# Kernel optimization log

Hardware: AMD Instinct MI355X
Metric: run time of the kernel (lower is better)

Reference implementation:

```python
import jax, jax.numpy as jnp
import numpy as np
import math

NUM_BUCKETS = 32
MAX_DISTANCE = 128

def _next_pow2(n):
    return 1 << (int(n) - 1).bit_length()

def _rel_pos_bucket(rel_pos):
    # causal T5 bucket: n = max(q - k, 0)
    n = jnp.maximum(-rel_pos, 0)
    max_exact = NUM_BUCKETS // 2
    is_small = n < max_exact
    n_safe = jnp.maximum(n, 1).astype(jnp.float32)
    val_if_large = max_exact + (
        jnp.log(n_safe / max_exact) / math.log(MAX_DISTANCE / max_exact) * (NUM_BUCKETS - max_exact)
    ).astype(jnp.int32)
    val_if_large = jnp.minimum(val_if_large, NUM_BUCKETS - 1)
    return jnp.where(is_small, n, val_if_large)

def setup_inputs() -> dict:
    key = jax.random.key(0)
    ks = jax.random.split(key, 20)
    B, L, D = 8, 2048, 128
    H, DQK, DV = 16, 64, 256
    s = 0.05
    return {
        'x': jax.random.normal(ks[0], (B, L, D), jnp.float32),
        'expansion': jax.random.normal(ks[1], (H, D), jnp.float32) * s,
        'reduction': jax.random.normal(ks[2], (H, D), jnp.float32) * s,
        'alphas': jax.random.normal(ks[3], (H,), jnp.float32),
        'dampen_factors': jax.random.normal(ks[4], (H,), jnp.float32),
        'rel_bias': jax.random.normal(ks[5], (NUM_BUCKETS, 1), jnp.float32) * s,
        'W_qk': jax.random.normal(ks[6], (D, DQK), jnp.float32) * s,
        'b_qk': jnp.zeros((DQK,), jnp.float32),
        'gamma': jax.random.normal(ks[7], (2, DQK), jnp.float32) * 0.02 + 1.0,
        'beta': jnp.zeros((2, DQK), jnp.float32),
        'W_v': jax.random.normal(ks[8], (D, DV), jnp.float32) * s,
        'b_v': jnp.zeros((DV,), jnp.float32),
        'W_reset': jax.random.normal(ks[9], (D, DV), jnp.float32) * s,
        'b_reset': jnp.zeros((DV,), jnp.float32),
        'W_update': jax.random.normal(ks[10], (D, D), jnp.float32) * s,
        'b_update': jnp.zeros((D,), jnp.float32),
        'Wh': jax.random.normal(ks[11], (D, D), jnp.float32) * s,
        'Uh': jax.random.normal(ks[12], (DV, D), jnp.float32) * s,
        'bh': jnp.zeros((D,), jnp.float32),
    }

def reference(x, expansion, reduction, alphas, dampen_factors, rel_bias,
              W_qk, b_qk, gamma, beta, W_v, b_v, W_reset, b_reset,
              W_update, b_update, Wh, Uh, bh):
    B, L, D = x.shape
    DQK = W_qk.shape[1]
    # ---- MultiHeadedEMA (causal, FFT conv) ----
    xe = jnp.einsum('bnd,hd->bnhd', x, expansion)  # [B,L,H,D]
    a = jax.nn.sigmoid(alphas)
    damp = jax.nn.sigmoid(dampen_factors)
    t = jnp.arange(L, dtype=x.dtype)
    kern = a[:, None] * ((1.0 - a) * damp)[:, None] ** t[None, :]  # [H,L]
    fft_len = _next_pow2(2 * L - 1)
    Xf = jnp.fft.rfft(xe, n=fft_len, axis=1)           # [B,F,H,D]
    Kf = jnp.fft.rfft(kern, n=fft_len, axis=-1)        # [H,F]
    y = jnp.fft.irfft(Xf * Kf.T[None, :, :, None], n=fft_len, axis=1)[:, :L]
    ema = jnp.einsum('bnhd,hd->bnd', y, reduction)     # [B,L,D]
    # ---- SingleHeadedAttention(ema, v_input=x) ----
    qk = jax.nn.silu(ema @ W_qk + b_qk)                # [B,L,DQK]
    q = qk * gamma[0] + beta[0]
    k = qk * gamma[1] + beta[1]
    v = jax.nn.silu(x @ W_v + b_v)                     # [B,L,DV]
    scale = D ** -0.5
    sim = jnp.einsum('bid,bjd->bij', q, k) * scale
    pos = jnp.arange(L)
    rel = pos[None, :] - pos[:, None]                  # [L,L] j - i
    bias = rel_bias[_rel_pos_bucket(rel), 0] * (DQK ** 0.5)
    sim = sim + bias
    sim = jnp.where(rel > 0, jnp.finfo(sim.dtype).min, sim)  # strict causal mask
    attn = jax.nn.softmax(sim, axis=-1)
    attn_out = jnp.einsum('bij,bjd->bid', attn, v)     # [B,L,DV]
    # ---- gating ----
    reset_gate = jax.nn.silu(ema @ W_reset + b_reset)
    update_gate = jax.nn.sigmoid(ema @ W_update + b_update)
    gated = attn_out * reset_gate
    Hh = jax.nn.silu(ema @ Wh + gated @ Uh + bh)
    return update_gate * Hh + (1.0 - update_gate) * x
```

## Files before the change

kernel.cpp:

```cpp
#include <hip/hip_runtime.h>
#include <hip/hip_bf16.h>
#include <math.h>

#define BB 8
#define LL 2048
#define DD 128
#define DQKN 64
#define DVN 256
#define MTOT (BB*LL)
#define SCALE 0.08838834764831845f
#define LOG2E 1.4426950408889634f
#define QSCALE (SCALE*LOG2E)

#define CHUNK 32
#define NCH (LL/CHUNK)
#define CT 4
#define NCHK 144

typedef __attribute__((ext_vector_type(4))) float f32x4;
typedef __attribute__((ext_vector_type(8))) short s16x8;

__device__ __forceinline__ float sigmoidf_(float x){ return 1.f/(1.f+__expf(-x)); }
__device__ __forceinline__ float siluf_(float x){ return x/(1.f+__expf(-x)); }
__device__ __forceinline__ __hip_bfloat16 f2bf(float f){ return __float2bfloat16(f); }
__device__ __forceinline__ ushort f2bfu(float f){ __hip_bfloat16 h = __float2bfloat16(f); return *(const ushort*)&h; }
__device__ __forceinline__ float bf2f(ushort u){ union{unsigned i; float f;} v; v.i = ((unsigned)u)<<16; return v.f; }

__device__ __forceinline__ void gl_lds16(const __hip_bfloat16* g, void* l) {
    __builtin_amdgcn_global_load_lds(
        (const __attribute__((address_space(1))) void*)g,
        (__attribute__((address_space(3))) void*)l, 16, 0, 0);
}

__global__ void pack_all(const float* __restrict__ Wqk, const float* __restrict__ Wv,
                         const float* __restrict__ Wrst, const float* __restrict__ Wu,
                         const float* __restrict__ Wh, const float* __restrict__ Uh,
                         const float* __restrict__ rel_bias,
                         __hip_bfloat16* __restrict__ WqkP, __hip_bfloat16* __restrict__ WvP,
                         __hip_bfloat16* __restrict__ WrstP, __hip_bfloat16* __restrict__ WuP,
                         __hip_bfloat16* __restrict__ WhP, __hip_bfloat16* __restrict__ UhP,
                         float* __restrict__ btab) {
    int blk = blockIdx.x;
    int l = threadIdx.x;
    if (blk == 272) {
        for (int n = l; n < LL; n += 64) {
            int bucket;
            if (n < 16) bucket = n;
            else {
                float v = logf((float)n * (1.0f/16.0f)) * (1.0f/logf(8.0f)) * 16.0f;
                bucket = 16 + (int)v;
                if (bucket > 31) bucket = 31;
            }
            btab[n] = rel_bias[bucket] * 8.0f * LOG2E;
        }
        return;
    }
    const float* W; __hip_bfloat16* Wp; int K, N;
    if (blk < 16)       { W=Wqk;  Wp=WqkP;  K=128; N=64; }
    else if (blk < 80)  { W=Wv;   Wp=WvP;   K=128; N=256; blk-=16; }
    else if (blk < 144) { W=Wrst; Wp=WrstP; K=128; N=256; blk-=80; }
    else if (blk < 176) { W=Wu;   Wp=WuP;   K=128; N=128; blk-=144; }
    else if (blk < 208) { W=Wh;   Wp=WhP;   K=128; N=128; blk-=176; }
    else                { W=Uh;   Wp=UhP;   K=256; N=128; blk-=208; }
    int k32 = blk % (K/32), n16 = blk / (K/32);
    int col = n16*16 + (l & 15);
    int krow = k32*32 + (l >> 4)*8;
    ushort tmp[8];
    #pragma unroll
    for (int j = 0; j < 8; ++j) tmp[j] = f2bfu(W[(size_t)(krow + j)*N + col]);
    *reinterpret_cast<uint4*>(Wp + ((size_t)blk*64 + l)*8) = *reinterpret_cast<uint4*>(tmp);
}

__global__ __launch_bounds__(256) void ema_scanA(const float* __restrict__ x,
                                                 const float* __restrict__ alphas,
                                                 const float* __restrict__ damps,
                                                 float* __restrict__ sl,
                                                 __hip_bfloat16* __restrict__ xb) {
    int tid = blockIdx.x * 256 + threadIdx.x;
    int d = tid & 127;
    int c = (tid >> 7) & (NCH - 1);
    int b = tid >> 13;
    float u[16], r[16];
    #pragma unroll
    for (int h = 0; h < 16; ++h) {
        float a = sigmoidf_(alphas[h]);
        r[h] = (1.f - a) * sigmoidf_(damps[h]);
        u[h] = 0.f;
    }
    const float* xp = x + ((size_t)b * LL + c * CHUNK) * DD + d;
    __hip_bfloat16* xbp = xb + ((size_t)b * LL + c * CHUNK) * DD + d;
    #pragma unroll 4
    for (int i = 0; i < CHUNK; ++i) {
        float xv = xp[(size_t)i * DD];
        xbp[(size_t)i * DD] = f2bf(xv);
        #pragma unroll
        for (int h = 0; h < 16; ++h) u[h] = fmaf(r[h], u[h], xv);
    }
    float* slp = sl + ((size_t)b * NCH + c) * 16 * DD + d;
    #pragma unroll
    for (int h = 0; h < 16; ++h) slp[(size_t)h * DD] = u[h];
}

__global__ __launch_bounds__(256) void ema_scanB(const float* __restrict__ alphas,
                                                 const float* __restrict__ damps,
                                                 const float* __restrict__ sl,
                                                 float* __restrict__ carry) {
    int tid = blockIdx.x * 256 + threadIdx.x;
    int d = tid & 127;
    int h = (tid >> 7) & 15;
    int b = tid >> 11;
    float a = sigmoidf_(alphas[h]);
    float r = (1.f - a) * sigmoidf_(damps[h]);
    float rC = r;
    #pragma unroll
    for (int q = 0; q < 5; ++q) rC *= rC;
    const float* slp = sl + ((size_t)b * NCH * 16 + h) * DD + d;
    float* cp = carry + ((size_t)b * NCH * 16 + h) * DD + d;
    float u = 0.f;
    #pragma unroll 8
    for (int c = 0; c < NCH; ++c) {
        cp[(size_t)c * 16 * DD] = u;
        u = slp[(size_t)c * 16 * DD] + rC * u;
    }
}

__global__ __launch_bounds__(256) void ema_scanC(const __hip_bfloat16* __restrict__ xb,
                                                 const float* __restrict__ expansion,
                                                 const float* __restrict__ reduction,
                                                 const float* __restrict__ alphas,
                                                 const float* __restrict__ damps,
                                                 const float* __restrict__ carry,
                                                 __hip_bfloat16* __restrict__ emab) {
    int tid = blockIdx.x * 256 + threadIdx.x;
    int d = tid & 127;
    int c = (tid >> 7) & (NCH - 1);
    int b = tid >> 13;
    float u[16], r[16], we[16];
    #pragma unroll
    for (int h = 0; h < 16; ++h) {
        float a = sigmoidf_(alphas[h]);
        r[h] = (1.f - a) * sigmoidf_(damps[h]);
        we[h] = reduction[h * DD + d] * a * expansion[h * DD + d];
        u[h] = carry[((size_t)b * NCH + c) * 16 * DD + (size_t)h * DD + d];
    }
    const __hip_bfloat16* xp = xb + ((size_t)b * LL + c * CHUNK) * DD + d;
    __hip_bfloat16* ep = emab + ((size_t)b * LL + c * CHUNK) * DD + d;
    #pragma unroll 4
    for (int i = 0; i < CHUNK; ++i) {
        float xv = __bfloat162float(xp[(size_t)i * DD]);
        float acc = 0.f;
        #pragma unroll
        for (int h = 0; h < 16; ++h) {
            u[h] = fmaf(r[h], u[h], xv);
            acc = fmaf(we[h], u[h], acc);
        }
        ep[(size_t)i * DD] = f2bf(acc);
    }
}

__global__ __launch_bounds__(256) void gemm_fused(const __hip_bfloat16* __restrict__ xb,
        const __hip_bfloat16* __restrict__ emab,
        const __hip_bfloat16* __restrict__ WvP, const __hip_bfloat16* __restrict__ WrstP,
        const __hip_bfloat16* __restrict__ WqkP,
        const float* __restrict__ b_v, const float* __restrict__ b_rst,
        const float* __restrict__ b_qk, const float* __restrict__ gamma,
        const float* __restrict__ beta,
        __hip_bfloat16* __restrict__ vT, __hip_bfloat16* __restrict__ rstb,
        __hip_bfloat16* __restrict__ qb, __hip_bfloat16* __restrict__ kb) {
    __shared__ char AsB[64*256];
    const int mode = blockIdx.y;
    const __hip_bfloat16* A = (mode == 0) ? xb : emab;
    const int row0 = blockIdx.x * 64;
    const int t = threadIdx.x, w = t>>6, lane = t&63, l16 = lane&15, l4 = lane>>4;
    #pragma unroll
    for (int p = 0; p < 4; ++p) {
        int idx = p*256 + t;
        int row = idx / 16, u = idx % 16;
        uint4 d = *reinterpret_cast<const uint4*>(A + (size_t)(row0+row)*DD + u*8);
        *reinterpret_cast<uint4*>(AsB + row*256 + ((u*16) ^ ((row&7)<<4))) = d;
    }
    __syncthreads();
    const int arow = w*16 + l16;
    if (mode == 2) {
        f32x4 acc[4];
        #pragma unroll
        for (int n = 0; n < 4; ++n) acc[n] = (f32x4){0.f,0.f,0.f,0.f};
        #pragma unroll
        for (int k32 = 0; k32 < 4; ++k32) {
            s16x8 af = *reinterpret_cast<const s16x8*>(AsB + arow*256 + ((k32*64 + l4*16) ^ ((arow&7)<<4)));
            #pragma unroll
            for (int n = 0; n < 4; ++n) {
                s16x8 bfr = *reinterpret_cast<const s16x8*>(WqkP + ((size_t)(n*4 + k32)*64 + lane)*8);
                acc[n] = __builtin_amdgcn_mfma_f32_16x16x32_bf16(af, bfr, acc[n], 0, 0, 0);
            }
        }
        #pragma unroll
        for (int n = 0; n < 4; ++n) {
            int col = n*16 + l16;
            float bb = b_qk[col];
            float g0 = gamma[col], g1 = gamma[DQKN + col];
            float be0 = beta[col], be1 = beta[DQKN + col];
            #pragma unroll
            for (int r = 0; r < 4; ++r) {
                int row = w*16 + l4*4 + r;
                float s = siluf_(acc[n][r] + bb);
                qb[(size_t)(row0+row)*DQKN + col] = f2bf((s*g0 + be0) * QSCALE);
                kb[(size_t)(row0+row)*DQKN + col] = f2bf(s*g1 + be1);
            }
        }
        return;
    }
    const __hip_bfloat16* Wp = mode ? WrstP : WvP;
    const float* bias = mode ? b_rst : b_v;
    f32x4 acc[16];
    #pragma unroll
    for (int n = 0; n < 16; ++n) acc[n] = (f32x4){0.f,0.f,0.f,0.f};
    #pragma unroll
    for (int k32 = 0; k32 < 4; ++k32) {
        s16x8 af = *reinterpret_cast<const s16x8*>(AsB + arow*256 + ((k32*64 + l4*16) ^ ((arow&7)<<4)));
        #pragma unroll
        for (int n = 0; n < 16; ++n) {
            s16x8 bfr = *reinterpret_cast<const s16x8*>(Wp + ((size_t)(n*4 + k32)*64 + lane)*8);
            acc[n] = __builtin_amdgcn_mfma_f32_16x16x32_bf16(af, bfr, acc[n], 0, 0, 0);
        }
    }
    if (mode == 0) {
        int bb_i = row0 >> 11;
        int lpos0 = (row0 & 2047) + w*16 + l4*4;
        #pragma unroll
        for (int n = 0; n < 16; ++n) {
            int col = n*16 + l16;
            float bb = bias[col];
            ushort pk[4];
            #pragma unroll
            for (int r = 0; r < 4; ++r) pk[r] = f2bfu(siluf_(acc[n][r] + bb));
            *reinterpret_cast<ushort4*>(vT + ((size_t)bb_i*DVN + col)*LL + lpos0) = *reinterpret_cast<ushort4*>(pk);
        }
    } else {
        #pragma unroll
        for (int n = 0; n < 16; ++n) {
            int col = n*16 + l16;
            float bb = bias[col];
            #pragma unroll
            for (int r = 0; r < 4; ++r) {
                int row = w*16 + l4*4 + r;
                rstb[(size_t)(row0+row)*DVN + col] = f2bf(siluf_(acc[n][r] + bb));
            }
        }
    }
}

__global__ __launch_bounds__(256) void attn_kernel(
    const __hip_bfloat16* __restrict__ qg, const __hip_bfloat16* __restrict__ kg,
    const __hip_bfloat16* __restrict__ vTg, const float* __restrict__ btab,
    __hip_bfloat16* __restrict__ aob, __hip_bfloat16* __restrict__ part_o,
    float* __restrict__ part_ml) {
    __shared__ __hip_bfloat16 Ks[64 * 64];
    __shared__ __hip_bfloat16 Vs[256 * 64];
    __shared__ __hip_bfloat16 Ps[4][16][72];
    __shared__ float btl[320];
    const int cid = NCHK - 1 - (int)blockIdx.y;
    const int b = blockIdx.x;
    int g = 0;
    while (cid >= 2*(g+1)*(g+2)) ++g;
    const int rel = cid - 2*g*(g+1);
    const int ti = 4*g + rel/(g+1);
    const int cch = rel % (g+1);
    const int i0 = ti * 64;
    const int jlo = cch * (CT*64);
    int jhi = jlo + CT*64; { int je = (ti+1)*64; if (jhi > je) jhi = je; }
    const int nt = (jhi - jlo) >> 6;
    const int t = threadIdx.x;
    const int w = t >> 6, lane = t & 63;
    const int l16 = lane & 15, l4 = lane >> 4;
    char* KsB = (char*)Ks;
    char* VsB = (char*)Vs;

    int dmin = i0 - jhi + 1; if (dmin < 0) dmin = 0;
    const int cnt = (i0 + 63 - jlo) - dmin + 1;
    for (int idx = t; idx < cnt; idx += 256) btl[idx] = btab[dmin + idx];

    const int irow = i0 + w * 16 + l16;
    s16x8 qf[2];
    qf[0] = *reinterpret_cast<const s16x8*>(qg + ((size_t)b * LL + irow) * DQKN + l4 * 8);
    qf[1] = *reinterpret_cast<const s16x8*>(qg + ((size_t)b * LL + irow) * DQKN + 32 + l4 * 8);

    f32x4 o[16];
    #pragma unroll
    for (int n16 = 0; n16 < 16; ++n16) o[n16] = (f32x4){0.f, 0.f, 0.f, 0.f};
    float m[4] = {-1e30f, -1e30f, -1e30f, -1e30f};
    float l[4] = {0.f, 0.f, 0.f, 0.f};

    for (int tt = 0; tt < nt; ++tt) {
        const int j0 = jlo + tt * 64;
        __syncthreads();
        #pragma unroll
        for (int i = 0; i < 2; ++i) {
            int base = w * 128 + i * 64;
            int idx = base + lane;
            int row = idx >> 3;
            int c16 = (idx & 7) ^ (row & 7);
            gl_lds16(kg + ((size_t)b * LL + j0 + row) * DQKN + c16 * 8, KsB + base * 16);
        }
        #pragma unroll
        for (int i = 0; i < 8; ++i) {
            int base = w * 512 + i * 64;
            int idx = base + lane;
            int n = idx >> 3;
            int c16 = (idx & 7) ^ (n & 7);
            gl_lds16(vTg + ((size_t)b * DVN + n) * LL + j0 + c16 * 8, VsB + base * 16);
        }
        __syncthreads();
        f32x4 s[4];
        #pragma unroll
        for (int t16 = 0; t16 < 4; ++t16) s[t16] = (f32x4){0.f, 0.f, 0.f, 0.f};
        #pragma unroll
        for (int c = 0; c < 2; ++c) {
            #pragma unroll
            for (int t16 = 0; t16 < 4; ++t16) {
                int j = t16 * 16 + l16;
                s16x8 kf = *reinterpret_cast<const s16x8*>(KsB + j * 128 + ((c * 64 + l4 * 16) ^ ((j & 7) << 4)));
                s[t16] = __builtin_amdgcn_mfma_f32_16x16x32_bf16(qf[c], kf, s[t16], 0, 0, 0);
            }
        }
        float sv[4][4];
        float rmax[4] = {-1e30f, -1e30f, -1e30f, -1e30f};
        #pragma unroll
        for (int t16 = 0; t16 < 4; ++t16) {
            #pragma unroll
            for (int r = 0; r < 4; ++r) {
                int row = l4 * 4 + r;
                int dlt = (i0 + w * 16 + row) - (j0 + t16 * 16 + l16);
                int bi = dlt - dmin; if (bi < 0) bi = 0;
                float bv = btl[bi];
                float val = (dlt >= 0) ? (s[t16][r] + bv) : -1e30f;
                sv[t16][r] = val;
                rmax[r] = fmaxf(rmax[r], val);
            }
        }
        #pragma unroll
        for (int off = 1; off < 16; off <<= 1) {
            #pragma unroll
            for (int r = 0; r < 4; ++r) rmax[r] = fmaxf(rmax[r], __shfl_xor(rmax[r], off));
        }
        bool need = (rmax[0] > m[0]) || (rmax[1] > m[1]) || (rmax[2] > m[2]) || (rmax[3] > m[3]);
        if (__any(need)) {
            float alpha[4];
            #pragma unroll
            for (int r = 0; r < 4; ++r) {
                float mn = fmaxf(m[r], rmax[r]);
                alpha[r] = exp2f(m[r] - mn);
                m[r] = mn;
                l[r] *= alpha[r];
            }
            #pragma unroll
            for (int n16 = 0; n16 < 16; ++n16) {
                #pragma unroll
                for (int r = 0; r < 4; ++r) o[n16][r] *= alpha[r];
            }
        }
        float psum[4] = {0.f, 0.f, 0.f, 0.f};
        #pragma unroll
        for (int t16 = 0; t16 < 4; ++t16) {
            #pragma unroll
            for (int r = 0; r < 4; ++r) {
                float p = exp2f(sv[t16][r] - m[r]);
                psum[r] += p;
                Ps[w][l4 * 4 + r][t16 * 16 + l16] = f2bf(p);
            }
        }
        #pragma unroll
        for (int off = 1; off < 16; off <<= 1) {
            #pragma unroll
            for (int r = 0; r < 4; ++r) psum[r] += __shfl_xor(psum[r], off);
        }
        #pragma unroll
        for (int r = 0; r < 4; ++r) l[r] += psum[r];
        #pragma unroll
        for (int c = 0; c < 2; ++c) {
            s16x8 pf = *reinterpret_cast<const s16x8*>(&Ps[w][l16][c * 32 + l4 * 8]);
            #pragma unroll
            for (int n16 = 0; n16 < 16; ++n16) {
                int n = n16 * 16 + l16;
                s16x8 vf = *reinterpret_cast<const s16x8*>(VsB + n * 128 + ((c * 64 + l4 * 16) ^ ((n & 7) << 4)));
                o[n16] = __builtin_amdgcn_mfma_f32_16x16x32_bf16(pf, vf, o[n16], 0, 0, 0);
            }
        }
    }
    if (ti < 4) {
        float invl[4];
        #pragma unroll
        for (int r = 0; r < 4; ++r) invl[r] = 1.f / l[r];
        #pragma unroll
        for (int n16 = 0; n16 < 16; ++n16) {
            #pragma unroll
            for (int r = 0; r < 4; ++r) {
                aob[((size_t)b * LL + i0 + w * 16 + l4 * 4 + r) * DVN + n16 * 16 + l16] = f2bf(o[n16][r] * invl[r]);
            }
        }
    } else {
        const size_t slot = (size_t)b * NCHK + cid;
        __hip_bfloat16* po = part_o + slot * (64 * 256);
        #pragma unroll
        for (int n16 = 0; n16 < 16; ++n16) {
            #pragma unroll
            for (int r = 0; r < 4; ++r)
                po[(size_t)(w * 16 + l4 * 4 + r) * 256 + n16 * 16 + l16] = f2bf(o[n16][r]);
        }
        if (l16 == 0) {
            #pragma unroll
            for (int r = 0; r < 4; ++r) {
                int row = w * 16 + l4 * 4 + r;
                part_ml[slot * 128 + row * 2]     = m[r];
                part_ml[slot * 128 + row * 2 + 1] = l[r];
            }
        }
    }
}

__global__ __launch_bounds__(256) void attn_combine(const __hip_bfloat16* __restrict__ part_o,
                                                    const float* __restrict__ part_ml,
                                                    __hip_bfloat16* __restrict__ aob) {
    const int ti = 4 + (int)blockIdx.x;
    const int ch = blockIdx.y;
    const int b = blockIdx.z;
    const int g = ti >> 2;
    const int nc = g + 1;
    const int cid0 = 2*g*(g+1) + (ti - 4*g)*(g+1);
    const size_t slot0 = (size_t)b * NCHK + cid0;
    __shared__ float sW[8][64];
    __shared__ float sinvL[64];
    const int t = threadIdx.x;
    if (t < 64) {
        float M = -1e30f;
        for (int c = 0; c < nc; ++c)
            M = fmaxf(M, part_ml[(slot0 + c) * 128 + t * 2]);
        float L = 0.f;
        for (int c = 0; c < nc; ++c) {
            float wv = exp2f(part_ml[(slot0 + c) * 128 + t * 2] - M);
            sW[c][t] = wv;
            L += wv * part_ml[(slot0 + c) * 128 + t * 2 + 1];
        }
        sinvL[t] = 1.f / L;
    }
    __syncthreads();
    const int i0 = ti * 64;
    #pragma unroll
    for (int it = 0; it < 4; ++it) {
        int idx = it * 256 + t;
        int row = idx >> 4, c8 = idx & 15;
        int colu = ch * 16 + c8;
        float acc[8] = {0.f,0.f,0.f,0.f,0.f,0.f,0.f,0.f};
        for (int c = 0; c < nc; ++c) {
            float wv = sW[c][row];
            uint4 d = *reinterpret_cast<const uint4*>(part_o + (slot0 + c) * (size_t)(64*256) + row * 256 + colu * 8);
            const ushort* pp = (const ushort*)&d;
            #pragma unroll
            for (int j = 0; j < 8; ++j) acc[j] = fmaf(wv, bf2f(pp[j]), acc[j]);
        }
        float il = sinvL[row];
        ushort pk[8];
        #pragma unroll
        for (int j = 0; j < 8; ++j) pk[j] = f2bfu(acc[j] * il);
        *reinterpret_cast<uint4*>(aob + ((size_t)b * LL + i0 + row) * DVN + colu * 8) = *reinterpret_cast<uint4*>(pk);
    }
}

__global__ __launch_bounds__(256) void final_mfma(
        const __hip_bfloat16* __restrict__ emab, const __hip_bfloat16* __restrict__ aob,
        const __hip_bfloat16* __restrict__ rstb, const float* __restrict__ x,
        const __hip_bfloat16* __restrict__ WhP, const __hip_bfloat16* __restrict__ UhP,
        const __hip_bfloat16* __restrict__ WuP, const float* __restrict__ bh,
        const float* __restrict__ bu, float* __restrict__ out) {
    __shared__ char As1[64*256];
    __shared__ char As2[64*512];
    const int row0 = blockIdx.x * 64;
    const int ch = blockIdx.y;
    const int t = threadIdx.x, w = t>>6, lane = t&63, l16 = lane&15, l4 = lane>>4;
    #pragma unroll
    for (int p = 0; p < 4; ++p) {
        int idx = p*256 + t;
        int row = idx / 16, u = idx % 16;
        uint4 d = *reinterpret_cast<const uint4*>(emab + (size_t)(row0+row)*DD + u*8);
        *reinterpret_cast<uint4*>(As1 + row*256 + ((u*16) ^ ((row&7)<<4))) = d;
    }
    #pragma unroll
    for (int p = 0; p < 8; ++p) {
        int idx = p*256 + t;
        int row = idx / 32, u = idx % 32;
        uint4 da = *reinterpret_cast<const uint4*>(aob + (size_t)(row0+row)*DVN + u*8);
        uint4 dr = *reinterpret_cast<const uint4*>(rstb + (size_t)(row0+row)*DVN + u*8);
        const ushort* pa = (const ushort*)&da;
        const ushort* pr = (const ushort*)&dr;
        ushort gg[8];
        #pragma unroll
        for (int j = 0; j < 8; ++j) gg[j] = f2bfu(bf2f(pa[j]) * bf2f(pr[j]));
        *reinterpret_cast<uint4*>(As2 + row*512 + ((u*16) ^ ((row&7)<<4))) = *reinterpret_cast<uint4*>(gg);
    }
    __syncthreads();
    f32x4 acc1[4], acc2[4];
    #pragma unroll
    for (int n = 0; n < 4; ++n) { acc1[n] = (f32x4){0.f,0.f,0.f,0.f}; acc2[n] = (f32x4){0.f,0.f,0.f,0.f}; }
    const int arow = w*16 + l16;
    #pragma unroll
    for (int k32 = 0; k32 < 4; ++k32) {
        s16x8 af = *reinterpret_cast<const s16x8*>(As1 + arow*256 + ((k32*64 + l4*16) ^ ((arow&7)<<4)));
        #pragma unroll
        for (int n = 0; n < 4; ++n) {
            s16x8 bw = *reinterpret_cast<const s16x8*>(WhP + ((size_t)((ch*4+n)*4 + k32)*64 + lane)*8);
            acc1[n] = __builtin_amdgcn_mfma_f32_16x16x32_bf16(af, bw, acc1[n], 0, 0, 0);
            s16x8 bu2 = *reinterpret_cast<const s16x8*>(WuP + ((size_t)((ch*4+n)*4 + k32)*64 + lane)*8);
            acc2[n] = __builtin_amdgcn_mfma_f32_16x16x32_bf16(af, bu2, acc2[n], 0, 0, 0);
        }
    }
    #pragma unroll
    for (int k32 = 0; k32 < 8; ++k32) {
        s16x8 gf = *reinterpret_cast<const s16x8*>(As2 + arow*512 + ((k32*64 + l4*16) ^ ((arow&7)<<4)));
        #pragma unroll
        for (int n = 0; n < 4; ++n) {
            s16x8 bw = *reinterpret_cast<const s16x8*>(UhP + ((size_t)((ch*4+n)*8 + k32)*64 + lane)*8);
            acc1[n] = __builtin_amdgcn_mfma_f32_16x16x32_bf16(gf, bw, acc1[n], 0, 0, 0);
        }
    }
    #pragma unroll
    for (int n = 0; n < 4; ++n) {
        int col = ch*64 + n*16 + l16;
        float bbh = bh[col], bbu = bu[col];
        #pragma unroll
        for (int r = 0; r < 4; ++r) {
            int row = w*16 + l4*4 + r;
            size_t gidx = (size_t)(row0+row)*DD + col;
            float hh = siluf_(acc1[n][r] + bbh);
            float u = sigmoidf_(acc2[n][r] + bbu);
            float xv = x[gidx];
            out[gidx] = u*hh + (1.f-u)*xv;
        }
    }
}

extern "C" void kernel_launch(void* const* d_in, const int* in_sizes, int n_in,
                              void* d_out, int out_size, void* d_ws, size_t ws_size,
                              hipStream_t stream) {
    const float* x        = (const float*)d_in[0];
    const float* expansion= (const float*)d_in[1];
    const float* reduction= (const float*)d_in[2];
    const float* alphas   = (const float*)d_in[3];
    const float* damps    = (const float*)d_in[4];
    const float* rel_bias = (const float*)d_in[5];
    const float* W_qk     = (const float*)d_in[6];
    const float* b_qk     = (const float*)d_in[7];
    const float* gamma    = (const float*)d_in[8];
    const float* beta     = (const float*)d_in[9];
    const float* W_v      = (const float*)d_in[10];
    const float* b_v      = (const float*)d_in[11];
    const float* W_reset  = (const float*)d_in[12];
    const float* b_reset  = (const float*)d_in[13];
    const float* W_update = (const float*)d_in[14];
    const float* b_update = (const float*)d_in[15];
    const float* Wh       = (const float*)d_in[16];
    const float* Uh       = (const float*)d_in[17];
    const float* bh       = (const float*)d_in[18];
    float* out = (float*)d_out;

    char* base = (char*)d_ws;
    __hip_bfloat16* emab = (__hip_bfloat16*)base;  base += (size_t)MTOT * DD * 2;
    __hip_bfloat16* xb   = (__hip_bfloat16*)base;  base += (size_t)MTOT * DD * 2;
    __hip_bfloat16* qb   = (__hip_bfloat16*)base;  base += (size_t)MTOT * DQKN * 2;
    __hip_bfloat16* kb   = (__hip_bfloat16*)base;  base += (size_t)MTOT * DQKN * 2;
    __hip_bfloat16* vT   = (__hip_bfloat16*)base;  base += (size_t)MTOT * DVN * 2;
    __hip_bfloat16* rstb = (__hip_bfloat16*)base;  base += (size_t)MTOT * DVN * 2;
    __hip_bfloat16* aob  = (__hip_bfloat16*)base;  base += (size_t)MTOT * DVN * 2;
    float* btab  = (float*)base;                   base += (size_t)LL * 4;
    float* sl    = (float*)base;                   base += (size_t)BB * NCH * 16 * DD * 4;
    float* carry = (float*)base;                   base += (size_t)BB * NCH * 16 * DD * 4;
    __hip_bfloat16* WqkP = (__hip_bfloat16*)base;  base += (size_t)DD * DQKN * 2;
    __hip_bfloat16* WvP  = (__hip_bfloat16*)base;  base += (size_t)DD * DVN * 2;
    __hip_bfloat16* WrstP= (__hip_bfloat16*)base;  base += (size_t)DD * DVN * 2;
    __hip_bfloat16* WuP  = (__hip_bfloat16*)base;  base += (size_t)DD * DD * 2;
    __hip_bfloat16* WhP  = (__hip_bfloat16*)base;  base += (size_t)DD * DD * 2;
    __hip_bfloat16* UhP  = (__hip_bfloat16*)base;  base += (size_t)DVN * DD * 2;
    __hip_bfloat16* part_o = (__hip_bfloat16*)base; base += (size_t)BB * NCHK * 64 * 256 * 2;
    float* part_ml = (float*)base;                 base += (size_t)BB * NCHK * 128 * 4;

    pack_all<<<273, 64, 0, stream>>>(W_qk, W_v, W_reset, W_update, Wh, Uh, rel_bias,
                                     WqkP, WvP, WrstP, WuP, WhP, UhP, btab);

    ema_scanA<<<BB * NCH * DD / 256, 256, 0, stream>>>(x, alphas, damps, sl, xb);
    ema_scanB<<<BB * 16 * DD / 256, 256, 0, stream>>>(alphas, damps, sl, carry);
    ema_scanC<<<BB * NCH * DD / 256, 256, 0, stream>>>(xb, expansion, reduction, alphas, damps, carry, emab);

    gemm_fused<<<dim3(MTOT/64, 3), 256, 0, stream>>>(xb, emab, WvP, WrstP, WqkP,
                                                     b_v, b_reset, b_qk, gamma, beta,
                                                     vT, rstb, qb, kb);

    attn_kernel<<<dim3(BB, NCHK), 256, 0, stream>>>(qb, kb, vT, btab, aob, part_o, part_ml);
    attn_combine<<<dim3(28, 2, BB), 256, 0, stream>>>(part_o, part_ml, aob);

    final_mfma<<<dim3(MTOT/64, 2), 256, 0, stream>>>(emab, aob, rstb, x, WhP, UhP, WuP, bh, b_update, out);
}
```

Before: 117.8 us.

## Fuse attention combine into final GEMM and merge weight packing with scan

Removes the separate attn_combine kernel and the aob intermediate. Every attention tile, including the first four that used to normalize in place, now writes partials, and the final kernel merges the split-K partials while it builds the gated operand. The final kernel also computes all 128 output columns per block instead of splitting columns across two blocks, so the emab/gate staging is not duplicated. Weight packing and the first EMA scan pass are merged into one launch. Together these cut kernel launches and a full bf16 round trip of the attention output, at the cost of fewer final blocks and more register pressure per block.

```diff
diff --git a/kernel.cpp b/kernel.cpp
--- a/kernel.cpp
+++ b/kernel.cpp
@@ -32,50 +32,52 @@
         (__attribute__((address_space(3))) void*)l, 16, 0, 0);
 }
 
-__global__ void pack_all(const float* __restrict__ Wqk, const float* __restrict__ Wv,
-                         const float* __restrict__ Wrst, const float* __restrict__ Wu,
-                         const float* __restrict__ Wh, const float* __restrict__ Uh,
-                         const float* __restrict__ rel_bias,
-                         __hip_bfloat16* __restrict__ WqkP, __hip_bfloat16* __restrict__ WvP,
-                         __hip_bfloat16* __restrict__ WrstP, __hip_bfloat16* __restrict__ WuP,
-                         __hip_bfloat16* __restrict__ WhP, __hip_bfloat16* __restrict__ UhP,
-                         float* __restrict__ btab) {
-    int blk = blockIdx.x;
-    int l = threadIdx.x;
-    if (blk == 272) {
-        for (int n = l; n < LL; n += 64) {
-            int bucket;
-            if (n < 16) bucket = n;
-            else {
-                float v = logf((float)n * (1.0f/16.0f)) * (1.0f/logf(8.0f)) * 16.0f;
-                bucket = 16 + (int)v;
-                if (bucket > 31) bucket = 31;
-            }
-            btab[n] = rel_bias[bucket] * 8.0f * LOG2E;
-        }
+__global__ __launch_bounds__(256) void prep_kernel(
+        const float* __restrict__ x, const float* __restrict__ alphas,
+        const float* __restrict__ damps, float* __restrict__ sl,
+        __hip_bfloat16* __restrict__ xb,
+        const float* __restrict__ Wqk, const float* __restrict__ Wv,
+        const float* __restrict__ Wrst, const float* __restrict__ Wu,
+        const float* __restrict__ Wh, const float* __restrict__ Uh,
+        const float* __restrict__ rel_bias,
+        __hip_bfloat16* __restrict__ WqkP, __hip_bfloat16* __restrict__ WvP,
+        __hip_bfloat16* __restrict__ WrstP, __hip_bfloat16* __restrict__ WuP,
+        __hip_bfloat16* __restrict__ WhP, __hip_bfloat16* __restrict__ UhP,
+        float* __restrict__ btab) {
+    if (blockIdx.x >= 256) {
+        int sub = ((int)blockIdx.x - 256) * 4 + ((int)threadIdx.x >> 6);
+        int l = threadIdx.x & 63;
+        if (sub >= 273) return;
+        if (sub == 272) {
+            for (int n = l; n < LL; n += 64) {
+                int bucket;
+                if (n < 16) bucket = n;
+                else {
+                    float v = logf((float)n * (1.0f/16.0f)) * (1.0f/logf(8.0f)) * 16.0f;
+                    bucket = 16 + (int)v;
+                    if (bucket > 31) bucket = 31;
+                }
+                btab[n] = rel_bias[bucket] * 8.0f * LOG2E;
+            }
+            return;
+        }
+        int blk = sub;
+        const float* W; __hip_bfloat16* Wp; int K, N;
+        if (blk < 16)       { W=Wqk;  Wp=WqkP;  K=128; N=64; }
+        else if (blk < 80)  { W=Wv;   Wp=WvP;   K=128; N=256; blk-=16; }
+        else if (blk < 144) { W=Wrst; Wp=WrstP; K=128; N=256; blk-=80; }
+        else if (blk < 176) { W=Wu;   Wp=WuP;   K=128; N=128; blk-=144; }
+        else if (blk < 208) { W=Wh;   Wp=WhP;   K=128; N=128; blk-=176; }
+        else                { W=Uh;   Wp=UhP;   K=256; N=128; blk-=208; }
+        int k32 = blk % (K/32), n16 = blk / (K/32);
+        int col = n16*16 + (l & 15);
+        int krow = k32*32 + (l >> 4)*8;
+        ushort tmp[8];
+        #pragma unroll
+        for (int j = 0; j < 8; ++j) tmp[j] = f2bfu(W[(size_t)(krow + j)*N + col]);
+        *reinterpret_cast<uint4*>(Wp + ((size_t)blk*64 + l)*8) = *reinterpret_cast<uint4*>(tmp);
         return;
     }
-    const float* W; __hip_bfloat16* Wp; int K, N;
-    if (blk < 16)       { W=Wqk;  Wp=WqkP;  K=128; N=64; }
-    else if (blk < 80)  { W=Wv;   Wp=WvP;   K=128; N=256; blk-=16; }
-    else if (blk < 144) { W=Wrst; Wp=WrstP; K=128; N=256; blk-=80; }
-    else if (blk < 176) { W=Wu;   Wp=WuP;   K=128; N=128; blk-=144; }
-    else if (blk < 208) { W=Wh;   Wp=WhP;   K=128; N=128; blk-=176; }
-    else                { W=Uh;   Wp=UhP;   K=256; N=128; blk-=208; }
-    int k32 = blk % (K/32), n16 = blk / (K/32);
-    int col = n16*16 + (l & 15);
-    int krow = k32*32 + (l >> 4)*8;
-    ushort tmp[8];
-    #pragma unroll
-    for (int j = 0; j < 8; ++j) tmp[j] = f2bfu(W[(size_t)(krow + j)*N + col]);
-    *reinterpret_cast<uint4*>(Wp + ((size_t)blk*64 + l)*8) = *reinterpret_cast<uint4*>(tmp);
-}
-
-__global__ __launch_bounds__(256) void ema_scanA(const float* __restrict__ x,
-                                                 const float* __restrict__ alphas,
-                                                 const float* __restrict__ damps,
-                                                 float* __restrict__ sl,
-                                                 __hip_bfloat16* __restrict__ xb) {
     int tid = blockIdx.x * 256 + threadIdx.x;
     int d = tid & 127;
     int c = (tid >> 7) & (NCH - 1);
@@ -253,8 +255,7 @@
 __global__ __launch_bounds__(256) void attn_kernel(
     const __hip_bfloat16* __restrict__ qg, const __hip_bfloat16* __restrict__ kg,
     const __hip_bfloat16* __restrict__ vTg, const float* __restrict__ btab,
-    __hip_bfloat16* __restrict__ aob, __hip_bfloat16* __restrict__ part_o,
-    float* __restrict__ part_ml) {
+    __hip_bfloat16* __restrict__ part_o, float* __restrict__ part_ml) {
     __shared__ __hip_bfloat16 Ks[64 * 64];
     __shared__ __hip_bfloat16 Vs[256 * 64];
     __shared__ __hip_bfloat16 Ps[4][16][72];
@@ -387,50 +388,43 @@
             }
         }
     }
-    if (ti < 4) {
-        float invl[4];
-        #pragma unroll
-        for (int r = 0; r < 4; ++r) invl[r] = 1.f / l[r];
-        #pragma unroll
-        for (int n16 = 0; n16 < 16; ++n16) {
-            #pragma unroll
-            for (int r = 0; r < 4; ++r) {
-                aob[((size_t)b * LL + i0 + w * 16 + l4 * 4 + r) * DVN + n16 * 16 + l16] = f2bf(o[n16][r] * invl[r]);
-            }
-        }
-    } else {
-        const size_t slot = (size_t)b * NCHK + cid;
-        __hip_bfloat16* po = part_o + slot * (64 * 256);
-        #pragma unroll
-        for (int n16 = 0; n16 < 16; ++n16) {
-            #pragma unroll
-            for (int r = 0; r < 4; ++r)
-                po[(size_t)(w * 16 + l4 * 4 + r) * 256 + n16 * 16 + l16] = f2bf(o[n16][r]);
-        }
-        if (l16 == 0) {
-            #pragma unroll
-            for (int r = 0; r < 4; ++r) {
-                int row = w * 16 + l4 * 4 + r;
-                part_ml[slot * 128 + row * 2]     = m[r];
-                part_ml[slot * 128 + row * 2 + 1] = l[r];
-            }
-        }
-    }
-}
-
-__global__ __launch_bounds__(256) void attn_combine(const __hip_bfloat16* __restrict__ part_o,
-                                                    const float* __restrict__ part_ml,
-                                                    __hip_bfloat16* __restrict__ aob) {
-    const int ti = 4 + (int)blockIdx.x;
-    const int ch = blockIdx.y;
-    const int b = blockIdx.z;
+    const size_t slot = (size_t)b * NCHK + cid;
+    __hip_bfloat16* po = part_o + slot * (64 * 256);
+    #pragma unroll
+    for (int n16 = 0; n16 < 16; ++n16) {
+        #pragma unroll
+        for (int r = 0; r < 4; ++r)
+            po[(size_t)(w * 16 + l4 * 4 + r) * 256 + n16 * 16 + l16] = f2bf(o[n16][r]);
+    }
+    if (l16 == 0) {
+        #pragma unroll
+        for (int r = 0; r < 4; ++r) {
+            int row = w * 16 + l4 * 4 + r;
+            part_ml[slot * 128 + row * 2]     = m[r];
+            part_ml[slot * 128 + row * 2 + 1] = l[r];
+        }
+    }
+}
+
+__global__ __launch_bounds__(256) void final_fused(
+        const __hip_bfloat16* __restrict__ part_o, const float* __restrict__ part_ml,
+        const __hip_bfloat16* __restrict__ emab, const __hip_bfloat16* __restrict__ rstb,
+        const float* __restrict__ x,
+        const __hip_bfloat16* __restrict__ WhP, const __hip_bfloat16* __restrict__ UhP,
+        const __hip_bfloat16* __restrict__ WuP, const float* __restrict__ bh,
+        const float* __restrict__ bu, float* __restrict__ out) {
+    __shared__ char As1[64*256];
+    __shared__ char As2[64*512];
+    __shared__ float sW[8][64];
+    __shared__ float sinvL[64];
+    const int row0 = blockIdx.x * 64;
+    const int b = blockIdx.x >> 5;
+    const int ti = blockIdx.x & 31;
     const int g = ti >> 2;
     const int nc = g + 1;
     const int cid0 = 2*g*(g+1) + (ti - 4*g)*(g+1);
     const size_t slot0 = (size_t)b * NCHK + cid0;
-    __shared__ float sW[8][64];
-    __shared__ float sinvL[64];
-    const int t = threadIdx.x;
+    const int t = threadIdx.x, w = t>>6, lane = t&63, l16 = lane&15, l4 = lane>>4;
     if (t < 64) {
         float M = -1e30f;
         for (int c = 0; c < nc; ++c)
@@ -443,40 +437,6 @@
         }
         sinvL[t] = 1.f / L;
     }
-    __syncthreads();
-    const int i0 = ti * 64;
-    #pragma unroll
-    for (int it = 0; it < 4; ++it) {
-        int idx = it * 256 + t;
-        int row = idx >> 4, c8 = idx & 15;
-        int colu = ch * 16 + c8;
-        float acc[8] = {0.f,0.f,0.f,0.f,0.f,0.f,0.f,0.f};
-        for (int c = 0; c < nc; ++c) {
-            float wv = sW[c][row];
-            uint4 d = *reinterpret_cast<const uint4*>(part_o + (slot0 + c) * (size_t)(64*256) + row * 256 + colu * 8);
-            const ushort* pp = (const ushort*)&d;
-            #pragma unroll
-            for (int j = 0; j < 8; ++j) acc[j] = fmaf(wv, bf2f(pp[j]), acc[j]);
-        }
-        float il = sinvL[row];
-        ushort pk[8];
-        #pragma unroll
-        for (int j = 0; j < 8; ++j) pk[j] = f2bfu(acc[j] * il);
-        *reinterpret_cast<uint4*>(aob + ((size_t)b * LL + i0 + row) * DVN + colu * 8) = *reinterpret_cast<uint4*>(pk);
-    }
-}
-
-__global__ __launch_bounds__(256) void final_mfma(
-        const __hip_bfloat16* __restrict__ emab, const __hip_bfloat16* __restrict__ aob,
-        const __hip_bfloat16* __restrict__ rstb, const float* __restrict__ x,
-        const __hip_bfloat16* __restrict__ WhP, const __hip_bfloat16* __restrict__ UhP,
-        const __hip_bfloat16* __restrict__ WuP, const float* __restrict__ bh,
-        const float* __restrict__ bu, float* __restrict__ out) {
-    __shared__ char As1[64*256];
-    __shared__ char As2[64*512];
-    const int row0 = blockIdx.x * 64;
-    const int ch = blockIdx.y;
-    const int t = threadIdx.x, w = t>>6, lane = t&63, l16 = lane&15, l4 = lane>>4;
     #pragma unroll
     for (int p = 0; p < 4; ++p) {
         int idx = p*256 + t;
@@ -484,32 +444,40 @@
         uint4 d = *reinterpret_cast<const uint4*>(emab + (size_t)(row0+row)*DD + u*8);
         *reinterpret_cast<uint4*>(As1 + row*256 + ((u*16) ^ ((row&7)<<4))) = d;
     }
+    __syncthreads();
     #pragma unroll
     for (int p = 0; p < 8; ++p) {
         int idx = p*256 + t;
         int row = idx / 32, u = idx % 32;
-        uint4 da = *reinterpret_cast<const uint4*>(aob + (size_t)(row0+row)*DVN + u*8);
+        float acc[8] = {0.f,0.f,0.f,0.f,0.f,0.f,0.f,0.f};
+        for (int c = 0; c < nc; ++c) {
+            float wv = sW[c][row];
+            uint4 d = *reinterpret_cast<const uint4*>(part_o + (slot0 + c) * (size_t)(64*256) + row * 256 + u * 8);
+            const ushort* pp = (const ushort*)&d;
+            #pragma unroll
+            for (int j = 0; j < 8; ++j) acc[j] = fmaf(wv, bf2f(pp[j]), acc[j]);
+        }
+        float il = sinvL[row];
         uint4 dr = *reinterpret_cast<const uint4*>(rstb + (size_t)(row0+row)*DVN + u*8);
-        const ushort* pa = (const ushort*)&da;
         const ushort* pr = (const ushort*)&dr;
         ushort gg[8];
         #pragma unroll
-        for (int j = 0; j < 8; ++j) gg[j] = f2bfu(bf2f(pa[j]) * bf2f(pr[j]));
+        for (int j = 0; j < 8; ++j) gg[j] = f2bfu(acc[j] * il * bf2f(pr[j]));
         *reinterpret_cast<uint4*>(As2 + row*512 + ((u*16) ^ ((row&7)<<4))) = *reinterpret_cast<uint4*>(gg);
     }
     __syncthreads();
-    f32x4 acc1[4], acc2[4];
-    #pragma unroll
-    for (int n = 0; n < 4; ++n) { acc1[n] = (f32x4){0.f,0.f,0.f,0.f}; acc2[n] = (f32x4){0.f,0.f,0.f,0.f}; }
+    f32x4 acc1[8], acc2[8];
+    #pragma unroll
+    for (int n = 0; n < 8; ++n) { acc1[n] = (f32x4){0.f,0.f,0.f,0.f}; acc2[n] = (f32x4){0.f,0.f,0.f,0.f}; }
     const int arow = w*16 + l16;
     #pragma unroll
     for (int k32 = 0; k32 < 4; ++k32) {
         s16x8 af = *reinterpret_cast<const s16x8*>(As1 + arow*256 + ((k32*64 + l4*16) ^ ((arow&7)<<4)));
         #pragma unroll
-        for (int n = 0; n < 4; ++n) {
-            s16x8 bw = *reinterpret_cast<const s16x8*>(WhP + ((size_t)((ch*4+n)*4 + k32)*64 + lane)*8);
+        for (int n = 0; n < 8; ++n) {
+            s16x8 bw = *reinterpret_cast<const s16x8*>(WhP + ((size_t)(n*4 + k32)*64 + lane)*8);
             acc1[n] = __builtin_amdgcn_mfma_f32_16x16x32_bf16(af, bw, acc1[n], 0, 0, 0);
-            s16x8 bu2 = *reinterpret_cast<const s16x8*>(WuP + ((size_t)((ch*4+n)*4 + k32)*64 + lane)*8);
+            s16x8 bu2 = *reinterpret_cast<const s16x8*>(WuP + ((size_t)(n*4 + k32)*64 + lane)*8);
             acc2[n] = __builtin_amdgcn_mfma_f32_16x16x32_bf16(af, bu2, acc2[n], 0, 0, 0);
         }
     }
@@ -517,14 +485,14 @@
     for (int k32 = 0; k32 < 8; ++k32) {
         s16x8 gf = *reinterpret_cast<const s16x8*>(As2 + arow*512 + ((k32*64 + l4*16) ^ ((arow&7)<<4)));
         #pragma unroll
-        for (int n = 0; n < 4; ++n) {
-            s16x8 bw = *reinterpret_cast<const s16x8*>(UhP + ((size_t)((ch*4+n)*8 + k32)*64 + lane)*8);
+        for (int n = 0; n < 8; ++n) {
+            s16x8 bw = *reinterpret_cast<const s16x8*>(UhP + ((size_t)(n*8 + k32)*64 + lane)*8);
             acc1[n] = __builtin_amdgcn_mfma_f32_16x16x32_bf16(gf, bw, acc1[n], 0, 0, 0);
         }
     }
     #pragma unroll
-    for (int n = 0; n < 4; ++n) {
-        int col = ch*64 + n*16 + l16;
+    for (int n = 0; n < 8; ++n) {
+        int col = n*16 + l16;
         float bbh = bh[col], bbu = bu[col];
         #pragma unroll
         for (int r = 0; r < 4; ++r) {
@@ -569,7 +537,6 @@
     __hip_bfloat16* kb   = (__hip_bfloat16*)base;  base += (size_t)MTOT * DQKN * 2;
     __hip_bfloat16* vT   = (__hip_bfloat16*)base;  base += (size_t)MTOT * DVN * 2;
     __hip_bfloat16* rstb = (__hip_bfloat16*)base;  base += (size_t)MTOT * DVN * 2;
-    __hip_bfloat16* aob  = (__hip_bfloat16*)base;  base += (size_t)MTOT * DVN * 2;
     float* btab  = (float*)base;                   base += (size_t)LL * 4;
     float* sl    = (float*)base;                   base += (size_t)BB * NCH * 16 * DD * 4;
     float* carry = (float*)base;                   base += (size_t)BB * NCH * 16 * DD * 4;
@@ -582,10 +549,10 @@
     __hip_bfloat16* part_o = (__hip_bfloat16*)base; base += (size_t)BB * NCHK * 64 * 256 * 2;
     float* part_ml = (float*)base;                 base += (size_t)BB * NCHK * 128 * 4;
 
-    pack_all<<<273, 64, 0, stream>>>(W_qk, W_v, W_reset, W_update, Wh, Uh, rel_bias,
-                                     WqkP, WvP, WrstP, WuP, WhP, UhP, btab);
-
-    ema_scanA<<<BB * NCH * DD / 256, 256, 0, stream>>>(x, alphas, damps, sl, xb);
+    prep_kernel<<<256 + 69, 256, 0, stream>>>(x, alphas, damps, sl, xb,
+                                              W_qk, W_v, W_reset, W_update, Wh, Uh, rel_bias,
+                                              WqkP, WvP, WrstP, WuP, WhP, UhP, btab);
+
     ema_scanB<<<BB * 16 * DD / 256, 256, 0, stream>>>(alphas, damps, sl, carry);
     ema_scanC<<<BB * NCH * DD / 256, 256, 0, stream>>>(xb, expansion, reduction, alphas, damps, carry, emab);
 
@@ -593,8 +560,8 @@
                                                      b_v, b_reset, b_qk, gamma, beta,
                                                      vT, rstb, qb, kb);
 
-    attn_kernel<<<dim3(BB, NCHK), 256, 0, stream>>>(qb, kb, vT, btab, aob, part_o, part_ml);
-    attn_combine<<<dim3(28, 2, BB), 256, 0, stream>>>(part_o, part_ml, aob);
-
-    final_mfma<<<dim3(MTOT/64, 2), 256, 0, stream>>>(emab, aob, rstb, x, WhP, UhP, WuP, bh, b_update, out);
-}
+    attn_kernel<<<dim3(BB, NCHK), 256, 0, stream>>>(qb, kb, vT, btab, part_o, part_ml);
+
+    final_fused<<<MTOT/64, 256, 0, stream>>>(part_o, part_ml, emab, rstb, x,
+                                             WhP, UhP, WuP, bh, b_update, out);
+}
```

Result: slower. 140.4 us (+19.2%).

## Double attention query tile to 128 rows with 512-thread blocks

Applied to the files above, without the earlier changes.

Each attention block now handles 128 query rows with 8 waves instead of 64 rows with 4 waves, so every K/V tile loaded into LDS is shared by twice as many query rows. The chunk enumeration, partial-result layout and combine kernel are rewritten for the new tile size, which halves the block count and the number of partial slots. The intent is to cut global K/V traffic and load overhead per query row. In exchange the grid has fewer, larger blocks, which may hurt occupancy and load balance, and diagonal tiles waste more masked work.

```diff
diff --git a/kernel.cpp b/kernel.cpp
--- a/kernel.cpp
+++ b/kernel.cpp
@@ -14,8 +14,9 @@
 
 #define CHUNK 32
 #define NCH (LL/CHUNK)
+#define QB 128
 #define CT 4
-#define NCHK 144
+#define NCHK 72
 
 typedef __attribute__((ext_vector_type(4))) float f32x4;
 typedef __attribute__((ext_vector_type(8))) short s16x8;
@@ -250,25 +251,23 @@
     }
 }
 
-__global__ __launch_bounds__(256) void attn_kernel(
+__global__ __launch_bounds__(512) void attn_kernel(
     const __hip_bfloat16* __restrict__ qg, const __hip_bfloat16* __restrict__ kg,
     const __hip_bfloat16* __restrict__ vTg, const float* __restrict__ btab,
     __hip_bfloat16* __restrict__ aob, __hip_bfloat16* __restrict__ part_o,
     float* __restrict__ part_ml) {
     __shared__ __hip_bfloat16 Ks[64 * 64];
     __shared__ __hip_bfloat16 Vs[256 * 64];
-    __shared__ __hip_bfloat16 Ps[4][16][72];
-    __shared__ float btl[320];
+    __shared__ __hip_bfloat16 Ps[8][16][72];
+    __shared__ float btl[384];
     const int cid = NCHK - 1 - (int)blockIdx.y;
     const int b = blockIdx.x;
-    int g = 0;
-    while (cid >= 2*(g+1)*(g+2)) ++g;
-    const int rel = cid - 2*g*(g+1);
-    const int ti = 4*g + rel/(g+1);
-    const int cch = rel % (g+1);
-    const int i0 = ti * 64;
+    int ti = 0, accu = 0;
+    while (cid >= accu + ((ti >> 1) + 1)) { accu += (ti >> 1) + 1; ++ti; }
+    const int cch = cid - accu;
+    const int i0 = ti * QB;
     const int jlo = cch * (CT*64);
-    int jhi = jlo + CT*64; { int je = (ti+1)*64; if (jhi > je) jhi = je; }
+    int jhi = jlo + CT*64; { int je = (ti+1)*QB; if (jhi > je) jhi = je; }
     const int nt = (jhi - jlo) >> 6;
     const int t = threadIdx.x;
     const int w = t >> 6, lane = t & 63;
@@ -277,8 +276,8 @@
     char* VsB = (char*)Vs;
 
     int dmin = i0 - jhi + 1; if (dmin < 0) dmin = 0;
-    const int cnt = (i0 + 63 - jlo) - dmin + 1;
-    for (int idx = t; idx < cnt; idx += 256) btl[idx] = btab[dmin + idx];
+    const int cnt = (i0 + QB - 1 - jlo) - dmin + 1;
+    for (int idx = t; idx < cnt; idx += 512) btl[idx] = btab[dmin + idx];
 
     const int irow = i0 + w * 16 + l16;
     s16x8 qf[2];
@@ -294,21 +293,17 @@
     for (int tt = 0; tt < nt; ++tt) {
         const int j0 = jlo + tt * 64;
         __syncthreads();
-        #pragma unroll
-        for (int i = 0; i < 2; ++i) {
-            int base = w * 128 + i * 64;
-            int idx = base + lane;
-            int row = idx >> 3;
-            int c16 = (idx & 7) ^ (row & 7);
-            gl_lds16(kg + ((size_t)b * LL + j0 + row) * DQKN + c16 * 8, KsB + base * 16);
-        }
-        #pragma unroll
-        for (int i = 0; i < 8; ++i) {
-            int base = w * 512 + i * 64;
-            int idx = base + lane;
+        {
+            int row = t >> 3;
+            int c16 = (t & 7) ^ (row & 7);
+            gl_lds16(kg + ((size_t)b * LL + j0 + row) * DQKN + c16 * 8, KsB + t * 16);
+        }
+        #pragma unroll
+        for (int i = 0; i < 4; ++i) {
+            int idx = i * 512 + t;
             int n = idx >> 3;
             int c16 = (idx & 7) ^ (n & 7);
-            gl_lds16(vTg + ((size_t)b * DVN + n) * LL + j0 + c16 * 8, VsB + base * 16);
+            gl_lds16(vTg + ((size_t)b * DVN + n) * LL + j0 + c16 * 8, VsB + idx * 16);
         }
         __syncthreads();
         f32x4 s[4];
@@ -387,7 +382,7 @@
             }
         }
     }
-    if (ti < 4) {
+    if (ti < 2) {
         float invl[4];
         #pragma unroll
         for (int r = 0; r < 4; ++r) invl[r] = 1.f / l[r];
@@ -400,7 +395,7 @@
         }
     } else {
         const size_t slot = (size_t)b * NCHK + cid;
-        __hip_bfloat16* po = part_o + slot * (64 * 256);
+        __hip_bfloat16* po = part_o + slot * (QB * 256);
         #pragma unroll
         for (int n16 = 0; n16 < 16; ++n16) {
             #pragma unroll
@@ -411,8 +406,8 @@
             #pragma unroll
             for (int r = 0; r < 4; ++r) {
                 int row = w * 16 + l4 * 4 + r;
-                part_ml[slot * 128 + row * 2]     = m[r];
-                part_ml[slot * 128 + row * 2 + 1] = l[r];
+                part_ml[slot * 256 + row * 2]     = m[r];
+                part_ml[slot * 256 + row * 2 + 1] = l[r];
             }
         }
     }
@@ -421,39 +416,39 @@
 __global__ __launch_bounds__(256) void attn_combine(const __hip_bfloat16* __restrict__ part_o,
                                                     const float* __restrict__ part_ml,
                                                     __hip_bfloat16* __restrict__ aob) {
-    const int ti = 4 + (int)blockIdx.x;
+    const int ti = 2 + (int)blockIdx.x;
     const int ch = blockIdx.y;
     const int b = blockIdx.z;
-    const int g = ti >> 2;
-    const int nc = g + 1;
-    const int cid0 = 2*g*(g+1) + (ti - 4*g)*(g+1);
+    const int k = ti >> 1;
+    const int nc = k + 1;
+    const int cid0 = (ti & 1) ? (k+1)*(k+1) : k*(k+1);
     const size_t slot0 = (size_t)b * NCHK + cid0;
-    __shared__ float sW[8][64];
-    __shared__ float sinvL[64];
+    __shared__ float sW[8][QB];
+    __shared__ float sinvL[QB];
     const int t = threadIdx.x;
-    if (t < 64) {
+    if (t < QB) {
         float M = -1e30f;
         for (int c = 0; c < nc; ++c)
-            M = fmaxf(M, part_ml[(slot0 + c) * 128 + t * 2]);
+            M = fmaxf(M, part_ml[(slot0 + c) * 256 + t * 2]);
         float L = 0.f;
         for (int c = 0; c < nc; ++c) {
-            float wv = exp2f(part_ml[(slot0 + c) * 128 + t * 2] - M);
+            float wv = exp2f(part_ml[(slot0 + c) * 256 + t * 2] - M);
             sW[c][t] = wv;
-            L += wv * part_ml[(slot0 + c) * 128 + t * 2 + 1];
+            L += wv * part_ml[(slot0 + c) * 256 + t * 2 + 1];
         }
         sinvL[t] = 1.f / L;
     }
     __syncthreads();
-    const int i0 = ti * 64;
-    #pragma unroll
-    for (int it = 0; it < 4; ++it) {
+    const int i0 = ti * QB;
+    #pragma unroll
+    for (int it = 0; it < 8; ++it) {
         int idx = it * 256 + t;
         int row = idx >> 4, c8 = idx & 15;
         int colu = ch * 16 + c8;
         float acc[8] = {0.f,0.f,0.f,0.f,0.f,0.f,0.f,0.f};
         for (int c = 0; c < nc; ++c) {
             float wv = sW[c][row];
-            uint4 d = *reinterpret_cast<const uint4*>(part_o + (slot0 + c) * (size_t)(64*256) + row * 256 + colu * 8);
+            uint4 d = *reinterpret_cast<const uint4*>(part_o + (slot0 + c) * (size_t)(QB*256) + row * 256 + colu * 8);
             const ushort* pp = (const ushort*)&d;
             #pragma unroll
             for (int j = 0; j < 8; ++j) acc[j] = fmaf(wv, bf2f(pp[j]), acc[j]);
@@ -579,8 +574,8 @@
     __hip_bfloat16* WuP  = (__hip_bfloat16*)base;  base += (size_t)DD * DD * 2;
     __hip_bfloat16* WhP  = (__hip_bfloat16*)base;  base += (size_t)DD * DD * 2;
     __hip_bfloat16* UhP  = (__hip_bfloat16*)base;  base += (size_t)DVN * DD * 2;
-    __hip_bfloat16* part_o = (__hip_bfloat16*)base; base += (size_t)BB * NCHK * 64 * 256 * 2;
-    float* part_ml = (float*)base;                 base += (size_t)BB * NCHK * 128 * 4;
+    __hip_bfloat16* part_o = (__hip_bfloat16*)base; base += (size_t)BB * NCHK * QB * 256 * 2;
+    float* part_ml = (float*)base;                 base += (size_t)BB * NCHK * 256 * 4;
 
     pack_all<<<273, 64, 0, stream>>>(W_qk, W_v, W_reset, W_update, Wh, Uh, rel_bias,
                                      WqkP, WvP, WrstP, WuP, WhP, UhP, btab);
@@ -593,8 +588,8 @@
                                                      b_v, b_reset, b_qk, gamma, beta,
                                                      vT, rstb, qb, kb);
 
-    attn_kernel<<<dim3(BB, NCHK), 256, 0, stream>>>(qb, kb, vT, btab, aob, part_o, part_ml);
-    attn_combine<<<dim3(28, 2, BB), 256, 0, stream>>>(part_o, part_ml, aob);
+    attn_kernel<<<dim3(BB, NCHK), 512, 0, stream>>>(qb, kb, vT, btab, aob, part_o, part_ml);
+    attn_combine<<<dim3(14, 2, BB), 256, 0, stream>>>(part_o, part_ml, aob);
 
     final_mfma<<<dim3(MTOT/64, 2), 256, 0, stream>>>(emab, aob, rstb, x, WhP, UhP, WuP, bh, b_update, out);
 }
```

After: 124.5 us. +5.7%, slower.
